# Kernel optimization log

Hardware: AMD Instinct MI355X
Metric: run time of the kernel (lower is better)

## Reference

```python
import jax, jax.numpy as jnp
import numpy as np

DIM = 768
TIME_DIM = 768
NUM_HEADS = 12
NUM_PATCHES = 784
GRID = 28  # sqrt(NUM_PATCHES)
REL_MAX = 2 * GRID - 1  # 55


def _rel_pos_indices():
    # Faithful to the torch buffer: relative_position_index = (dh + g-1) + (dw + g-1)
    coords = np.stack(np.meshgrid(np.arange(GRID), np.arange(GRID), indexing='ij'))  # [2,g,g]
    cf = coords.reshape(2, -1)  # [2,N]
    rel = cf[:, :, None] - cf[:, None, :]  # [2,N,N]
    rel = rel.transpose(1, 2, 0)
    rel[:, :, 0] += GRID - 1
    rel[:, :, 1] += GRID - 1
    idx = rel.sum(-1)  # [N,N], values in [0, 2*(2g-2)]
    # forward then splits this summed index (as written in the source):
    ih = idx // REL_MAX
    iw = idx % REL_MAX
    return jnp.asarray(ih, jnp.int32), jnp.asarray(iw, jnp.int32)


def setup_inputs() -> dict:
    key = jax.random.key(0)
    ks = jax.random.split(key, 16)
    B = 8
    s = 0.02
    inp = {
        'x_s': jax.random.normal(ks[0], (B, NUM_PATCHES, DIM), jnp.float32),
        'x_t': jax.random.normal(ks[1], (B, TIME_DIM), jnp.float32),
        'Wqs': jax.random.normal(ks[2], (DIM, DIM), jnp.float32) * s,
        'Wqt': jax.random.normal(ks[3], (TIME_DIM, DIM), jnp.float32) * s,
        'Wks': jax.random.normal(ks[4], (DIM, DIM), jnp.float32) * s,
        'Wkt': jax.random.normal(ks[5], (TIME_DIM, DIM), jnp.float32) * s,
        'Wvs': jax.random.normal(ks[6], (DIM, DIM), jnp.float32) * s,
        'Wvt': jax.random.normal(ks[7], (TIME_DIM, DIM), jnp.float32) * s,
        'rpb_table': jax.random.normal(ks[8], (REL_MAX, REL_MAX, NUM_HEADS), jnp.float32) * s,
        'proj_w': jax.random.normal(ks[9], (DIM, DIM), jnp.float32) * s,
        'proj_b': jnp.zeros((DIM,), jnp.float32),
    }
    return inp


def reference(x_s, x_t, Wqs, Wqt, Wks, Wkt, Wvs, Wvt, rpb_table, proj_w, proj_b):
    B, N, D = x_s.shape
    H = NUM_HEADS
    hd = D // H
    scale = hd ** -0.5

    # time-embed fused QKV: q = x_s @ Wqs + x_t @ Wqt (broadcast over tokens)
    q = x_s @ Wqs + (x_t @ Wqt)[:, None, :]
    k = x_s @ Wks + (x_t @ Wkt)[:, None, :]
    v = x_s @ Wvs + (x_t @ Wvt)[:, None, :]

    q = q.reshape(B, N, H, hd).transpose(0, 2, 1, 3)  # [B,H,N,hd]
    k = k.reshape(B, N, H, hd).transpose(0, 2, 1, 3)
    v = v.reshape(B, N, H, hd).transpose(0, 2, 1, 3)

    attn = jnp.einsum('bhnd,bhmd->bhnm', q, k) * scale  # [B,H,N,N]

    ih, iw = _rel_pos_indices()  # [N,N] each
    bias = rpb_table[ih, iw]  # [N,N,H]
    attn = attn + bias.transpose(2, 0, 1)[None]  # [1,H,N,N]

    attn = jax.nn.softmax(attn, axis=-1)
    x = jnp.einsum('bhnm,bhmd->bhnd', attn, v)
    x = x.transpose(0, 2, 1, 3).reshape(B, N, D)
    return x @ proj_w + proj_b
```

## Files before the change

kernel.cpp:

```cpp
#include <hip/hip_runtime.h>
#include <hip/hip_bf16.h>
#include <stdint.h>

#define DIM 768
#define NP  784
#define NH  12
#define HD  64
#define BATCH 8
#define MROWS (BATCH*NP)
#define MPAD 832
#define NCHUNK 32
#define KCH 24
#define L2E 1.4426950408889634f

using bf16x8 = __attribute__((ext_vector_type(8))) short;
using bf16x4 = __attribute__((ext_vector_type(4))) short;
using f32x4  = __attribute__((ext_vector_type(4))) float;

__device__ __forceinline__ short f2bf(float f) {
  union { float f; uint32_t u; } c; c.f = f;
  uint32_t u = c.u;
  u += 0x7FFFu + ((u >> 16) & 1u);
  return (short)(u >> 16);
}

__device__ __forceinline__ short bfr(float x) {
  union { __hip_bfloat16 b; short s; } u;
  u.b = __float2bfloat16(x);
  return u.s;
}

__device__ __forceinline__ void gld_lds16(const void* g, void* l) {
  __builtin_amdgcn_global_load_lds((const __attribute__((address_space(1))) uint32_t*)g,
                                   (__attribute__((address_space(3))) uint32_t*)l,
                                   16, 0, 0);
}

__global__ __launch_bounds__(256) void cvt_bf16_kernel(const float* __restrict__ src,
                                                       short* __restrict__ dst, int n8) {
  int i = blockIdx.x * 256 + threadIdx.x;
  if (i >= n8) return;
  const float4* s = (const float4*)src;
  float4 a = s[2*i], b = s[2*i+1];
  bf16x8 o;
  o[0]=f2bf(a.x); o[1]=f2bf(a.y); o[2]=f2bf(a.z); o[3]=f2bf(a.w);
  o[4]=f2bf(b.x); o[5]=f2bf(b.y); o[6]=f2bf(b.z); o[7]=f2bf(b.w);
  ((bf16x8*)dst)[i] = o;
}

__global__ __launch_bounds__(256) void wtrans_kernel(const float* __restrict__ w0,
                                                     const float* __restrict__ w1,
                                                     const float* __restrict__ w2,
                                                     const float* __restrict__ w3,
                                                     short* __restrict__ dst) {
  __shared__ float tile[32][33];
  const int z = blockIdx.z;
  const float* src = (z==0) ? w0 : (z==1) ? w1 : (z==2) ? w2 : w3;
  short* d = dst + (size_t)z * DIM * DIM;
  const int n0 = blockIdx.x*32, k0 = blockIdx.y*32;
  const int tx = threadIdx.x, ty = threadIdx.y;
#pragma unroll
  for (int i=0;i<4;i++) tile[ty+i*8][tx] = src[(size_t)(k0+ty+i*8)*DIM + n0+tx];
  __syncthreads();
#pragma unroll
  for (int i=0;i<4;i++) d[(size_t)(n0+ty+i*8)*DIM + k0+tx] = f2bf(tile[tx][ty+i*8]);
}

__global__ __launch_bounds__(256) void tvec1_kernel(const float* __restrict__ x_t,
                                                    const float* __restrict__ wq,
                                                    const float* __restrict__ wk,
                                                    const float* __restrict__ wv,
                                                    float* __restrict__ part) {
  const int z = blockIdx.x, kc = blockIdx.y;
  const float* w = (z==0) ? wq : (z==1) ? wk : wv;
  const int d = threadIdx.x;
  __shared__ float xs[BATCH][KCH];
  if (threadIdx.x < BATCH*KCH)
    xs[threadIdx.x / KCH][threadIdx.x % KCH] =
        x_t[(size_t)(threadIdx.x / KCH)*DIM + kc*KCH + threadIdx.x % KCH];
  __syncthreads();
  float a0[BATCH] = {}, a1[BATCH] = {}, a2[BATCH] = {};
#pragma unroll 4
  for (int k = 0; k < KCH; ++k) {
    const float* wr = w + (size_t)(kc*KCH + k)*DIM + d;
    float w0 = wr[0], w1 = wr[256], w2 = wr[512];
#pragma unroll
    for (int b = 0; b < BATCH; ++b) {
      float xv = xs[b][k];
      a0[b] += xv*w0; a1[b] += xv*w1; a2[b] += xv*w2;
    }
  }
#pragma unroll
  for (int b = 0; b < BATCH; ++b) {
    float* p = part + (((size_t)z*NCHUNK + kc)*BATCH + b)*DIM + d;
    p[0] = a0[b]; p[256] = a1[b]; p[512] = a2[b];
  }
}

__global__ __launch_bounds__(256) void tvec2_kernel(const float* __restrict__ part,
                                                    float* __restrict__ t) {
  const int i = blockIdx.x*256 + threadIdx.x;
  if (i >= 3*BATCH*DIM) return;
  const int z = i / (BATCH*DIM), rem = i % (BATCH*DIM);
  float s = 0.f;
#pragma unroll 8
  for (int c = 0; c < NCHUNK; ++c)
    s += part[((size_t)z*NCHUNK + c)*BATCH*DIM + rem];
  t[i] = s;
}

template<int MODE>
__global__ __launch_bounds__(256) void gemm_kernel(const short* __restrict__ A,
                                                   const short* __restrict__ Bw,
                                                   const float* __restrict__ aux,
                                                   short* __restrict__ outq,
                                                   short* __restrict__ outk,
                                                   short* __restrict__ outv,
                                                   float* __restrict__ outf) {
  __shared__ short As[128*32];
  __shared__ short Bs[128*32];
  const int bx = blockIdx.x, by = blockIdx.y, z = blockIdx.z;
  const short* Bz = Bw + (size_t)z * DIM * DIM;
  const int tid = threadIdx.x, w = tid>>6, lane = tid&63;
  const int wr = w>>1, wc = w&1, ln15 = lane&15, lg = lane>>4;
  const int m0 = by*128, n0 = bx*128;

  f32x4 acc[4][4] = {};

  for (int kt=0; kt<24; ++kt) {
    const int k0 = kt*32;
    __syncthreads();
#pragma unroll
    for (int i=0;i<2;i++) {
      const int inst = w*2 + i;
      const int off  = inst*1024 + lane*16;
      const int row  = off >> 6;
      const int ce   = (off & 63) >> 1;
      gld_lds16(A  + (size_t)(m0+row)*DIM + k0 + ce, (char*)As + (size_t)inst*1024);
      gld_lds16(Bz + (size_t)(n0+row)*DIM + k0 + ce, (char*)Bs + (size_t)inst*1024);
    }
    __syncthreads();
    bf16x8 af[4], bfr_[4];
#pragma unroll
    for (int mi=0;mi<4;mi++) af[mi]   = *(const bf16x8*)&As[(wr*64+mi*16+ln15)*32 + lg*8];
#pragma unroll
    for (int ni=0;ni<4;ni++) bfr_[ni] = *(const bf16x8*)&Bs[(wc*64+ni*16+ln15)*32 + lg*8];
#pragma unroll
    for (int mi=0;mi<4;mi++)
#pragma unroll
      for (int ni=0;ni<4;ni++)
        acc[mi][ni] = __builtin_amdgcn_mfma_f32_16x16x32_bf16(af[mi], bfr_[ni], acc[mi][ni], 0,0,0);
  }

  if (MODE == 0) {
    const float scl = (z==0) ? 0.125f * L2E : 1.0f;
#pragma unroll
    for (int mi=0;mi<4;mi++) {
#pragma unroll
      for (int j=0;j<4;j++) {
        const int r  = m0 + wr*64 + mi*16 + lg*4 + j;
        const int bb = r / NP;
        const int m  = r - bb*NP;
        const float* tv = aux + ((size_t)z*BATCH + bb) * DIM;
        if (z == 0) {
#pragma unroll
          for (int ni=0;ni<4;ni++) {
            const int gcol = n0 + wc*64 + ni*16 + ln15;
            outq[(size_t)r*DIM + gcol] = f2bf((acc[mi][ni][j] + tv[gcol]) * scl);
          }
        } else if (z == 1) {
#pragma unroll
          for (int ni=0;ni<4;ni++) {
            const int gcol = n0 + wc*64 + ni*16 + ln15;
            const int h = gcol >> 6, d = gcol & 63;
            outk[((size_t)(bb*NH + h)*MPAD + m)*HD + d] = f2bf(acc[mi][ni][j] + tv[gcol]);
          }
        }
      }
      if (MODE == 0 && z == 2) {
        const int r0 = m0 + wr*64 + mi*16 + lg*4;
        const int bb = r0 / NP;
        const int m  = r0 - bb*NP;
        const float* tv = aux + ((size_t)2*BATCH + bb) * DIM;
#pragma unroll
        for (int ni=0;ni<4;ni++) {
          const int gcol = n0 + wc*64 + ni*16 + ln15;
          const int h = gcol >> 6, d = gcol & 63;
          const float tb = tv[gcol];
          bf16x4 ov;
          ov[0] = f2bf(acc[mi][ni][0] + tb);
          ov[1] = f2bf(acc[mi][ni][1] + tb);
          ov[2] = f2bf(acc[mi][ni][2] + tb);
          ov[3] = f2bf(acc[mi][ni][3] + tb);
          *(bf16x4*)&outv[((size_t)(bb*NH + h)*HD + d)*MPAD + m] = ov;
        }
      }
    }
  } else {
#pragma unroll
    for (int mi=0;mi<4;mi++)
#pragma unroll
      for (int j=0;j<4;j++) {
        const int r = m0 + wr*64 + mi*16 + lg*4 + j;
#pragma unroll
        for (int ni=0;ni<4;ni++) {
          const int gcol = n0 + wc*64 + ni*16 + ln15;
          outf[(size_t)r*DIM + gcol] = acc[mi][ni][j] + aux[gcol];
        }
      }
  }
}

__global__ __launch_bounds__(512) void attn4_kernel(const short* __restrict__ Qb,
                                                    const short* __restrict__ Kt,
                                                    const short* __restrict__ Vt,
                                                    const float* __restrict__ rpb,
                                                    short* __restrict__ Ob) {
  __shared__ short kt[2][4096];
  __shared__ short vt[2][4096];
  __shared__ float4 bias4[112];
  const int hw = blockIdx.x;
  const int lgid = (hw & 7) * 84 + (hw >> 3);
  const int qt = lgid % 7;
  const int bh = lgid / 7;
  const int h = bh % NH, b = bh / NH;
  const int q0 = qt*128, tid = threadIdx.x, w = tid >> 6, lane = tid & 63;
  const int ln15 = lane & 15, lg = lane >> 4;

  if (tid < 112) {
    float4 v;
#pragma unroll
    for (int j = 0; j < 4; ++j) {
      const int i = tid - j - 2;
      float bv = 0.f;
      if (i >= 0 && i < 109)
        bv = rpb[(i/55)*(55*NH) + (i%55)*NH + h] * L2E;
      ((float*)&v)[j] = bv;
    }
    bias4[tid] = v;
  }

  const bool active = (q0 + w*16) < NP;
  const int q_idx = q0 + w*16 + ln15;
  bf16x8 qf0 = {}, qf1 = {};
  if (active) {
    const short* qp = Qb + ((size_t)(b*NP) + q_idx)*DIM + h*HD + lg*8;
    qf0 = *(const bf16x8*)qp;
    qf1 = *(const bf16x8*)(qp + 32);
  }
  const int qs56 = q_idx/28 + q_idx%28 + 56;

  const int lr = lane >> 3, lc = lane & 7;
  const int swe = (lc ^ lr) << 3;
  const size_t bhs = (size_t)bh;
  const short* kp0 = Kt + (bhs*MPAD + (size_t)(w*8 + lr))*HD + swe;
  const short* vp0 = Vt + (bhs*HD + (size_t)(w*8 + lr))*MPAD + swe;

#define STAGE2(BUF) { \
    gld_lds16(kp0, (char*)kt[BUF] + w*1024); \
    gld_lds16(vp0, (char*)vt[BUF] + w*1024); \
    kp0 += 64*HD; vp0 += 64; }

  float m_run = -3.0e38f, l_run = 0.f;
  f32x4 o0 = {}, o1 = {}, o2 = {}, o3 = {};

  STAGE2(0)

  for (int t = 0; t < 13; ++t) {
    const int cur = t & 1;
    const int m0 = t * 64;
    __syncthreads();
    if (t < 12) STAGE2(cur^1)
    if (active) {
      const char* kb = (const char*)kt[cur];
      const int sw = (ln15 & 7) << 4;
      f32x4 s[4];
#pragma unroll
      for (int mc = 0; mc < 4; ++mc) {
        const int rb = (mc*16 + ln15) * 128;
        bf16x8 kf0 = *(const bf16x8*)(kb + rb + ((lg*16) ^ sw));
        bf16x8 kf1 = *(const bf16x8*)(kb + rb + ((lg*16 + 64) ^ sw));
        f32x4 acc = {};
        acc = __builtin_amdgcn_mfma_f32_16x16x32_bf16(kf0, qf0, acc, 0,0,0);
        acc = __builtin_amdgcn_mfma_f32_16x16x32_bf16(kf1, qf1, acc, 0,0,0);
        s[mc] = acc;
      }
#pragma unroll
      for (int mc = 0; mc < 4; ++mc) {
        const int mb = m0 + mc*16 + lg*4;
        const int a28 = (mb * 2341) >> 16;
        const int idx0 = qs56 - mb + 27*a28;
        const float4 b4 = bias4[idx0];
        s[mc][0] += b4.x;
        s[mc][1] += b4.y;
        s[mc][2] += b4.z;
        s[mc][3] += b4.w;
      }
      if (m0 + 64 > NP) {
#pragma unroll
        for (int mc = 0; mc < 4; ++mc)
#pragma unroll
          for (int j = 0; j < 4; ++j)
            if (m0 + mc*16 + lg*4 + j >= NP) s[mc][j] = -1e30f;
      }
      float t0 = fmaxf(fmaxf(s[0][0],s[0][1]), fmaxf(s[0][2],s[0][3]));
      float t1 = fmaxf(fmaxf(s[1][0],s[1][1]), fmaxf(s[1][2],s[1][3]));
      float t2 = fmaxf(fmaxf(s[2][0],s[2][1]), fmaxf(s[2][2],s[2][3]));
      float t3 = fmaxf(fmaxf(s[3][0],s[3][1]), fmaxf(s[3][2],s[3][3]));
      float tm = fmaxf(fmaxf(t0,t1), fmaxf(t2,t3));
      tm = fmaxf(tm, __shfl_xor(tm, 16));
      tm = fmaxf(tm, __shfl_xor(tm, 32));
      const bool grow = !__all(tm - m_run <= 8.0f);
      float m_new = m_run, f = 1.0f;
      if (grow) { m_new = fmaxf(m_run, tm); f = exp2f(m_run - m_new); }
      float ts = 0.f;
#pragma unroll
      for (int mc = 0; mc < 4; ++mc) {
        float p0 = exp2f(s[mc][0]-m_new), p1 = exp2f(s[mc][1]-m_new);
        float p2 = exp2f(s[mc][2]-m_new), p3 = exp2f(s[mc][3]-m_new);
        s[mc][0]=p0; s[mc][1]=p1; s[mc][2]=p2; s[mc][3]=p3;
        ts += (p0+p1)+(p2+p3);
      }
      ts += __shfl_xor(ts, 16);
      ts += __shfl_xor(ts, 32);
      if (grow) {
        l_run = l_run * f + ts;
        m_run = m_new;
        o0 *= f; o1 *= f; o2 *= f; o3 *= f;
      } else {
        l_run += ts;
      }
      bf16x4 pb[4];
#pragma unroll
      for (int mc = 0; mc < 4; ++mc) {
        pb[mc][0] = bfr(s[mc][0]); pb[mc][1] = bfr(s[mc][1]);
        pb[mc][2] = bfr(s[mc][2]); pb[mc][3] = bfr(s[mc][3]);
      }
      const char* vb = (const char*)vt[cur];
#pragma unroll
      for (int mc = 0; mc < 4; ++mc) {
        const int ib = (mc*32 + lg*8) ^ sw;
        bf16x4 vf0 = *(const bf16x4*)(vb + (0*16+ln15)*128 + ib);
        bf16x4 vf1 = *(const bf16x4*)(vb + (1*16+ln15)*128 + ib);
        bf16x4 vf2 = *(const bf16x4*)(vb + (2*16+ln15)*128 + ib);
        bf16x4 vf3 = *(const bf16x4*)(vb + (3*16+ln15)*128 + ib);
        o0 = __builtin_amdgcn_mfma_f32_16x16x16bf16_1k(vf0, pb[mc], o0, 0,0,0);
        o1 = __builtin_amdgcn_mfma_f32_16x16x16bf16_1k(vf1, pb[mc], o1, 0,0,0);
        o2 = __builtin_amdgcn_mfma_f32_16x16x16bf16_1k(vf2, pb[mc], o2, 0,0,0);
        o3 = __builtin_amdgcn_mfma_f32_16x16x16bf16_1k(vf3, pb[mc], o3, 0,0,0);
      }
    }
  }
#undef STAGE2

  if (active) {
    const float inv = 1.0f / l_run;
    short* op = Ob + ((size_t)(b*NP) + q_idx)*DIM + h*HD + lg*4;
    bf16x4 ov;
    ov[0]=bfr(o0[0]*inv); ov[1]=bfr(o0[1]*inv); ov[2]=bfr(o0[2]*inv); ov[3]=bfr(o0[3]*inv);
    *(bf16x4*)(op + 0*16) = ov;
    ov[0]=bfr(o1[0]*inv); ov[1]=bfr(o1[1]*inv); ov[2]=bfr(o1[2]*inv); ov[3]=bfr(o1[3]*inv);
    *(bf16x4*)(op + 1*16) = ov;
    ov[0]=bfr(o2[0]*inv); ov[1]=bfr(o2[1]*inv); ov[2]=bfr(o2[2]*inv); ov[3]=bfr(o2[3]*inv);
    *(bf16x4*)(op + 2*16) = ov;
    ov[0]=bfr(o3[0]*inv); ov[1]=bfr(o3[1]*inv); ov[2]=bfr(o3[2]*inv); ov[3]=bfr(o3[3]*inv);
    *(bf16x4*)(op + 3*16) = ov;
  }
}

extern "C" void kernel_launch(void* const* d_in, const int* in_sizes, int n_in,
                              void* d_out, int out_size, void* d_ws, size_t ws_size,
                              hipStream_t stream) {
  const float* x_s = (const float*)d_in[0];
  const float* x_t = (const float*)d_in[1];
  const float* Wqs = (const float*)d_in[2];
  const float* Wqt = (const float*)d_in[3];
  const float* Wks = (const float*)d_in[4];
  const float* Wkt = (const float*)d_in[5];
  const float* Wvs = (const float*)d_in[6];
  const float* Wvt = (const float*)d_in[7];
  const float* rpb = (const float*)d_in[8];
  const float* pw  = (const float*)d_in[9];
  const float* pb  = (const float*)d_in[10];
  float* out = (float*)d_out;

  char* ws = (char*)d_ws;
  size_t off = 0;
  float* t_part = (float*)(ws + off); off += (size_t)3*NCHUNK*BATCH*DIM*4;
  float* t_vec  = (float*)(ws + off); off += (size_t)3*BATCH*DIM*4;
  short* Wt     = (short*)(ws + off); off += (size_t)4*DIM*DIM*2;
  short* Qb     = (short*)(ws + off); off += (size_t)MROWS*DIM*2;
  short* Ob     = (short*)(ws + off); off += (size_t)MROWS*DIM*2;
  short* Xb     = (short*)(ws + off); off += (size_t)MROWS*DIM*2;
  short* Kt     = (short*)(ws + off); off += (size_t)BATCH*NH*MPAD*HD*2;
  short* Vt     = (short*)(ws + off); off += (size_t)BATCH*NH*MPAD*HD*2;

  cvt_bf16_kernel<<<2352, 256, 0, stream>>>(x_s, Xb, MROWS*DIM/8);
  wtrans_kernel<<<dim3(24,24,4), dim3(32,8), 0, stream>>>(Wqs, Wks, Wvs, pw, Wt);
  tvec1_kernel<<<dim3(3,NCHUNK), 256, 0, stream>>>(x_t, Wqt, Wkt, Wvt, t_part);
  tvec2_kernel<<<72, 256, 0, stream>>>(t_part, t_vec);
  gemm_kernel<0><<<dim3(6,49,3), 256, 0, stream>>>(Xb, Wt, t_vec, Qb, Kt, Vt, nullptr);
  attn4_kernel<<<672, 512, 0, stream>>>(Qb, Kt, Vt, rpb, Ob);
  gemm_kernel<1><<<dim3(6,49,1), 256, 0, stream>>>(Ob, Wt + (size_t)3*DIM*DIM, pb,
                                                   nullptr, nullptr, nullptr, out);
}
```

Before: 134.2 us.

## Replace QKV GEMM with 256x256-tile double-buffered swizzled MFMA kernel

Adds a dedicated QKV projection kernel that uses 256x256 output tiles with 512 threads and a K-step of 64. LDS is double-buffered with async global-to-LDS loads, a swizzled LDS layout and s_setprio around the MFMA blocks. The goal is more data reuse per tile, fewer barriers, and overlap of loads with compute compared to the old 128x128, K=32, single-buffered GEMM. The cost is a partial last M tile: the grid rises to 25 row blocks, the Xb buffer is padded by 256 rows, and stores are bounds-checked. The grid also shrinks to 225 large blocks, which may leave the device underfilled.

```diff
diff --git a/kernel.cpp b/kernel.cpp
--- a/kernel.cpp
+++ b/kernel.cpp
@@ -109,18 +109,143 @@
   t[i] = s;
 }
 
+__global__ __launch_bounds__(512, 1) void qkv256_kernel(const short* __restrict__ A,
+                                                        const short* __restrict__ Wt,
+                                                        const float* __restrict__ aux,
+                                                        short* __restrict__ outq,
+                                                        short* __restrict__ outk,
+                                                        short* __restrict__ outv) {
+  __shared__ short As[2][256*64];
+  __shared__ short Bs[2][256*64];
+  const int bx = blockIdx.x, by = blockIdx.y;
+  const int z = bx / 3;
+  const int n0z = (bx - z*3) * 256;
+  const short* Bz = Wt + (size_t)z * DIM * DIM;
+  const int m0 = by * 256;
+  const int tid = threadIdx.x, w = tid >> 6, lane = tid & 63;
+  const int wr = w >> 2, wc = w & 3, ln15 = lane & 15, lg = lane >> 4;
+
+  const int lr8 = lane >> 3, c8e = (lane & 7) * 8;
+  const int swe = c8e ^ (lr8 << 3);
+  const short* aS = A  + (size_t)(m0  + w*8 + lr8) * DIM + swe;
+  const short* bS = Bz + (size_t)(n0z + w*8 + lr8) * DIM + swe;
+
+#define STG(TT, BSEL) { \
+    char* da = (char*)As[BSEL] + w*1024; \
+    char* db = (char*)Bs[BSEL] + w*1024; \
+    const int kk = (TT)*64; \
+    gld_lds16(aS + (size_t)0*64*DIM + kk, da + 0*8192); \
+    gld_lds16(bS + (size_t)0*64*DIM + kk, db + 0*8192); \
+    gld_lds16(aS + (size_t)1*64*DIM + kk, da + 1*8192); \
+    gld_lds16(bS + (size_t)1*64*DIM + kk, db + 1*8192); \
+    gld_lds16(aS + (size_t)2*64*DIM + kk, da + 2*8192); \
+    gld_lds16(bS + (size_t)2*64*DIM + kk, db + 2*8192); \
+    gld_lds16(aS + (size_t)3*64*DIM + kk, da + 3*8192); \
+    gld_lds16(bS + (size_t)3*64*DIM + kk, db + 3*8192); }
+
+  f32x4 acc[8][4] = {};
+
+  STG(0, 0)
+  STG(1, 1)
+
+  for (int t = 0; t < 12; ++t) {
+    const int cur = t & 1;
+    if (t < 11) asm volatile("s_waitcnt vmcnt(8)" ::: "memory");
+    else        asm volatile("s_waitcnt vmcnt(0)" ::: "memory");
+    __builtin_amdgcn_s_barrier();
+    const short* Ab = As[cur];
+    const short* Bb = Bs[cur];
+    bf16x8 bf[4], af[4];
+#pragma unroll
+    for (int ks = 0; ks < 2; ++ks) {
+#pragma unroll
+      for (int mh = 0; mh < 2; ++mh) {
+        if (mh == 0) {
+#pragma unroll
+          for (int ni = 0; ni < 4; ++ni) {
+            const int row = wc*64 + ni*16 + ln15;
+            bf[ni] = *(const bf16x8*)&Bb[row*64 + ((ks*32 + lg*8) ^ ((row & 7) << 3))];
+          }
+        }
+#pragma unroll
+        for (int mi = 0; mi < 4; ++mi) {
+          const int row = wr*128 + mh*64 + mi*16 + ln15;
+          af[mi] = *(const bf16x8*)&Ab[row*64 + ((ks*32 + lg*8) ^ ((row & 7) << 3))];
+        }
+        __builtin_amdgcn_s_barrier();
+        __builtin_amdgcn_s_setprio(1);
+#pragma unroll
+        for (int mi = 0; mi < 4; ++mi)
+#pragma unroll
+          for (int ni = 0; ni < 4; ++ni)
+            acc[mh*4+mi][ni] =
+                __builtin_amdgcn_mfma_f32_16x16x32_bf16(af[mi], bf[ni], acc[mh*4+mi][ni], 0,0,0);
+        __builtin_amdgcn_s_setprio(0);
+      }
+    }
+    __builtin_amdgcn_s_barrier();
+    if (t < 10) {
+      if (cur == 0) STG(t+2, 0)
+      else          STG(t+2, 1)
+    }
+  }
+
+  const float scl = 0.125f * L2E;
+#pragma unroll
+  for (int ai = 0; ai < 8; ++ai) {
+    const int rb = m0 + wr*128 + (ai>>2)*64 + (ai&3)*16 + lg*4;
+    if (z == 2) {
+      if (rb < MROWS) {
+        const int bb = rb / NP;
+        const int m  = rb - bb*NP;
+        const float* tv = aux + ((size_t)2*BATCH + bb) * DIM;
+#pragma unroll
+        for (int ni = 0; ni < 4; ++ni) {
+          const int col = n0z + wc*64 + ni*16 + ln15;
+          const int h = col >> 6, d = col & 63;
+          const float tb = tv[col];
+          bf16x4 ov;
+          ov[0] = f2bf(acc[ai][ni][0] + tb);
+          ov[1] = f2bf(acc[ai][ni][1] + tb);
+          ov[2] = f2bf(acc[ai][ni][2] + tb);
+          ov[3] = f2bf(acc[ai][ni][3] + tb);
+          *(bf16x4*)&outv[((size_t)(bb*NH + h)*HD + d)*MPAD + m] = ov;
+        }
+      }
+    } else {
+#pragma unroll
+      for (int j = 0; j < 4; ++j) {
+        const int r = rb + j;
+        if (r < MROWS) {
+          const int bb = r / NP;
+          const int m  = r - bb*NP;
+          const float* tv = aux + ((size_t)z*BATCH + bb) * DIM;
+#pragma unroll
+          for (int ni = 0; ni < 4; ++ni) {
+            const int col = n0z + wc*64 + ni*16 + ln15;
+            if (z == 0) {
+              outq[(size_t)r*DIM + col] = f2bf((acc[ai][ni][j] + tv[col]) * scl);
+            } else {
+              const int h = col >> 6, d = col & 63;
+              outk[((size_t)(bb*NH + h)*MPAD + m)*HD + d] = f2bf(acc[ai][ni][j] + tv[col]);
+            }
+          }
+        }
+      }
+    }
+  }
+#undef STG
+}
+
 template<int MODE>
 __global__ __launch_bounds__(256) void gemm_kernel(const short* __restrict__ A,
                                                    const short* __restrict__ Bw,
                                                    const float* __restrict__ aux,
-                                                   short* __restrict__ outq,
-                                                   short* __restrict__ outk,
-                                                   short* __restrict__ outv,
                                                    float* __restrict__ outf) {
   __shared__ short As[128*32];
   __shared__ short Bs[128*32];
-  const int bx = blockIdx.x, by = blockIdx.y, z = blockIdx.z;
-  const short* Bz = Bw + (size_t)z * DIM * DIM;
+  const int bx = blockIdx.x, by = blockIdx.y;
+  const short* Bz = Bw;
   const int tid = threadIdx.x, w = tid>>6, lane = tid&63;
   const int wr = w>>1, wc = w&1, ln15 = lane&15, lg = lane>>4;
   const int m0 = by*128, n0 = bx*128;
@@ -152,63 +277,17 @@
         acc[mi][ni] = __builtin_amdgcn_mfma_f32_16x16x32_bf16(af[mi], bfr_[ni], acc[mi][ni], 0,0,0);
   }
 
-  if (MODE == 0) {
-    const float scl = (z==0) ? 0.125f * L2E : 1.0f;
-#pragma unroll
-    for (int mi=0;mi<4;mi++) {
-#pragma unroll
-      for (int j=0;j<4;j++) {
-        const int r  = m0 + wr*64 + mi*16 + lg*4 + j;
-        const int bb = r / NP;
-        const int m  = r - bb*NP;
-        const float* tv = aux + ((size_t)z*BATCH + bb) * DIM;
-        if (z == 0) {
-#pragma unroll
-          for (int ni=0;ni<4;ni++) {
-            const int gcol = n0 + wc*64 + ni*16 + ln15;
-            outq[(size_t)r*DIM + gcol] = f2bf((acc[mi][ni][j] + tv[gcol]) * scl);
-          }
-        } else if (z == 1) {
-#pragma unroll
-          for (int ni=0;ni<4;ni++) {
-            const int gcol = n0 + wc*64 + ni*16 + ln15;
-            const int h = gcol >> 6, d = gcol & 63;
-            outk[((size_t)(bb*NH + h)*MPAD + m)*HD + d] = f2bf(acc[mi][ni][j] + tv[gcol]);
-          }
-        }
-      }
-      if (MODE == 0 && z == 2) {
-        const int r0 = m0 + wr*64 + mi*16 + lg*4;
-        const int bb = r0 / NP;
-        const int m  = r0 - bb*NP;
-        const float* tv = aux + ((size_t)2*BATCH + bb) * DIM;
-#pragma unroll
-        for (int ni=0;ni<4;ni++) {
-          const int gcol = n0 + wc*64 + ni*16 + ln15;
-          const int h = gcol >> 6, d = gcol & 63;
-          const float tb = tv[gcol];
-          bf16x4 ov;
-          ov[0] = f2bf(acc[mi][ni][0] + tb);
-          ov[1] = f2bf(acc[mi][ni][1] + tb);
-          ov[2] = f2bf(acc[mi][ni][2] + tb);
-          ov[3] = f2bf(acc[mi][ni][3] + tb);
-          *(bf16x4*)&outv[((size_t)(bb*NH + h)*HD + d)*MPAD + m] = ov;
-        }
-      }
-    }
-  } else {
-#pragma unroll
-    for (int mi=0;mi<4;mi++)
-#pragma unroll
-      for (int j=0;j<4;j++) {
-        const int r = m0 + wr*64 + mi*16 + lg*4 + j;
-#pragma unroll
-        for (int ni=0;ni<4;ni++) {
-          const int gcol = n0 + wc*64 + ni*16 + ln15;
-          outf[(size_t)r*DIM + gcol] = acc[mi][ni][j] + aux[gcol];
-        }
-      }
-  }
+#pragma unroll
+  for (int mi=0;mi<4;mi++)
+#pragma unroll
+    for (int j=0;j<4;j++) {
+      const int r = m0 + wr*64 + mi*16 + lg*4 + j;
+#pragma unroll
+      for (int ni=0;ni<4;ni++) {
+        const int gcol = n0 + wc*64 + ni*16 + ln15;
+        outf[(size_t)r*DIM + gcol] = acc[mi][ni][j] + aux[gcol];
+      }
+    }
 }
 
 __global__ __launch_bounds__(512) void attn4_kernel(const short* __restrict__ Qb,
@@ -391,7 +470,7 @@
   short* Wt     = (short*)(ws + off); off += (size_t)4*DIM*DIM*2;
   short* Qb     = (short*)(ws + off); off += (size_t)MROWS*DIM*2;
   short* Ob     = (short*)(ws + off); off += (size_t)MROWS*DIM*2;
-  short* Xb     = (short*)(ws + off); off += (size_t)MROWS*DIM*2;
+  short* Xb     = (short*)(ws + off); off += (size_t)(MROWS+256)*DIM*2;
   short* Kt     = (short*)(ws + off); off += (size_t)BATCH*NH*MPAD*HD*2;
   short* Vt     = (short*)(ws + off); off += (size_t)BATCH*NH*MPAD*HD*2;
 
@@ -399,8 +478,7 @@
   wtrans_kernel<<<dim3(24,24,4), dim3(32,8), 0, stream>>>(Wqs, Wks, Wvs, pw, Wt);
   tvec1_kernel<<<dim3(3,NCHUNK), 256, 0, stream>>>(x_t, Wqt, Wkt, Wvt, t_part);
   tvec2_kernel<<<72, 256, 0, stream>>>(t_part, t_vec);
-  gemm_kernel<0><<<dim3(6,49,3), 256, 0, stream>>>(Xb, Wt, t_vec, Qb, Kt, Vt, nullptr);
+  qkv256_kernel<<<dim3(9,25), 512, 0, stream>>>(Xb, Wt, t_vec, Qb, Kt, Vt);
   attn4_kernel<<<672, 512, 0, stream>>>(Qb, Kt, Vt, rpb, Ob);
-  gemm_kernel<1><<<dim3(6,49,1), 256, 0, stream>>>(Ob, Wt + (size_t)3*DIM*DIM, pb,
-                                                   nullptr, nullptr, nullptr, out);
-}
+  gemm_kernel<1><<<dim3(6,49,1), 256, 0, stream>>>(Ob, Wt + (size_t)3*DIM*DIM, pb, out);
+}
```

Result: slower. 140.8 us (+4.9%).
